# Optimization experiments

Hardware: AMD Instinct MI355X
Metric: run time of the kernel (lower is better)

The kernel has to match this reference:

```python
import jax, jax.numpy as jnp
import numpy as np

NUM_HEADS = 16
DIM = 1024
N_TOKENS = 2048
S0 = 8            # number of frames
P = N_TOKENS // S0  # tokens per frame
B = 1


def setup_inputs() -> dict:
    key = jax.random.key(0)
    ks = jax.random.split(key, 8)
    C = DIM
    x = jax.random.normal(ks[0], (B, N_TOKENS, C), dtype=jnp.float32)
    # nn.Linear-style weights (out_features, in_features), scaled ~1/sqrt(fan_in)
    Wqkv = jax.random.normal(ks[1], (3 * C, C), dtype=jnp.float32) * (C ** -0.5)
    bqkv = jnp.zeros((3 * C,), dtype=jnp.float32)
    Wproj = jax.random.normal(ks[2], (C, C), dtype=jnp.float32) * (C ** -0.5)
    bproj = jnp.zeros((C,), dtype=jnp.float32)
    frame_bias = jax.random.normal(ks[3], (S0, S0), dtype=jnp.float32) * 0.5
    # frame adjacency: random sparsity pattern, diagonal always allowed
    adj = jax.random.bernoulli(ks[4], 0.25, (S0, S0))
    adj = adj | jnp.eye(S0, dtype=bool)
    frame_ids = (jnp.arange(N_TOKENS) // P).astype(jnp.int64)
    is_hub = jax.random.bernoulli(ks[5], 0.05, (N_TOKENS,))
    return {
        'x': x, 'Wqkv': Wqkv, 'bqkv': bqkv, 'Wproj': Wproj, 'bproj': bproj,
        'frame_bias': frame_bias, 'adj': adj, 'frame_ids': frame_ids,
        'is_hub': is_hub,
    }


def _sparse_attention(x, Wqkv, bqkv, Wproj, bproj, frame_bias, adj, frame_ids, is_hub):
    Bx, N, C = x.shape
    H = NUM_HEADS
    D = C // H
    scale = D ** -0.5
    # qkv projection -> q,k,v each [B,H,N,D]
    qkv = x @ Wqkv.T + bqkv                      # [B,N,3C]
    qkv = qkv.reshape(Bx, N, 3, H, D).transpose(2, 0, 3, 1, 4)
    q, k, v = qkv[0], qkv[1], qkv[2]

    # token-level mask derived from frame-level structures (score_mod semantics)
    fi = frame_ids                               # [N]
    adj_allowed = adj[fi[:, None], fi[None, :]]  # [N,N] bool
    same_frame = fi[:, None] == fi[None, :]
    neither_hub = ~(is_hub[:, None] | is_hub[None, :])
    hub_allowed = same_frame | neither_hub       # mask_hub_tokens=True
    allowed = adj_allowed & hub_allowed
    bias = frame_bias[fi[:, None], fi[None, :]]  # soft_mask=True

    scores = jnp.einsum('bhqd,bhkd->bhqk', q, k) * scale
    scores = jnp.where(allowed, scores + bias, -jnp.inf)
    attn = jax.nn.softmax(scores, axis=-1)
    out = jnp.einsum('bhqk,bhkd->bhqd', attn, v)
    out = out.transpose(0, 2, 1, 3).reshape(Bx, N, C)
    return out @ Wproj.T + bproj


def reference(x, Wqkv, bqkv, Wproj, bproj, frame_bias, adj, frame_ids, is_hub):
    return _sparse_attention(x, Wqkv, bqkv, Wproj, bproj, frame_bias,
                             adj, frame_ids, is_hub)
```

## Files before the change

### kernel.cpp

```cpp
#include <hip/hip_runtime.h>
#include <hip/hip_bf16.h>
#include <math.h>

#define NTOK 2048
#define CDIM 1024
#define NHEAD 16
#define HDIM 64

typedef __attribute__((ext_vector_type(8))) short bf16x8;
typedef __attribute__((ext_vector_type(4))) short bf16x4;
typedef __attribute__((ext_vector_type(4))) float f32x4;
typedef __attribute__((ext_vector_type(4))) unsigned int u32x4;

__device__ inline unsigned short bf16_rn(float f) {
    unsigned int u = __float_as_uint(f);
    u += 0x7FFFu + ((u >> 16) & 1u);
    return (unsigned short)(u >> 16);
}

template <int N> __device__ inline void waitcnt_vm() {
    if constexpr (N == 0) asm volatile("s_waitcnt vmcnt(0)" ::: "memory");
    else if constexpr (N == 3) asm volatile("s_waitcnt vmcnt(3)" ::: "memory");
    else if constexpr (N == 4) asm volatile("s_waitcnt vmcnt(4)" ::: "memory");
}

__device__ inline void gload16(const void* g, void* l) {
    __builtin_amdgcn_global_load_lds((const __attribute__((address_space(1))) void*)g,
                                     (__attribute__((address_space(3))) void*)l,
                                     16, 0, 0);
}

__global__ __launch_bounds__(256) void conv3(const float* __restrict__ s0, unsigned short* __restrict__ h0, int nb0,
                                             const float* __restrict__ s1, unsigned short* __restrict__ h1, int nb1,
                                             const float* __restrict__ s2, unsigned short* __restrict__ h2) {
    int b = blockIdx.x;
    const float* s;
    unsigned short* hh;
    if (b < nb0) { s = s0; hh = h0; }
    else if (b < nb0 + nb1) { s = s1; hh = h1; b -= nb0; }
    else { s = s2; hh = h2; b -= nb0 + nb1; }
    const int i = b * 256 + threadIdx.x;
    float4 v = ((const float4*)s)[i];
    ushort4 h;
    h.x = bf16_rn(v.x); h.y = bf16_rn(v.y); h.z = bf16_rn(v.z); h.w = bf16_rn(v.w);
    ((ushort4*)hh)[i] = h;
}

template <int BM, int BN, int M, int N, int K, int MODE>
__global__ __launch_bounds__(256) void gemm_mfma(const unsigned short* __restrict__ Ah,
                                                 const unsigned short* __restrict__ Bh,
                                                 const float* __restrict__ bias,
                                                 float* __restrict__ C,
                                                 unsigned short* __restrict__ qg,
                                                 unsigned short* __restrict__ kg,
                                                 unsigned short* __restrict__ vtg) {
    constexpr int FM = BM / 32;
    constexpr int FN = BN / 32;
    constexpr int ASZ = BM * 32;
    constexpr int BSZ = BN * 32;
    constexpr int BUF = ASZ + BSZ;
    __shared__ unsigned short lds[2 * BUF];

    const int tid = threadIdx.x;
    const int lane = tid & 63;
    const int w = tid >> 6;
    const int m0 = blockIdx.y * BM;
    const int n0 = blockIdx.x * BN;
    const int wave_m = (w >> 1) * (BM / 2);
    const int wave_n = (w & 1) * (BN / 2);
    const int lr = lane & 15;
    const int kg_ = lane >> 4;
    const int srow = tid >> 2;
    const int scol = (tid & 3) * 8;

    const size_t aRow = (size_t)(m0 + srow) * K + scol;
    const size_t bRow = (size_t)(n0 + srow) * K + scol;

    f32x4 acc[FM][FN];
#pragma unroll
    for (int i = 0; i < FM; ++i)
#pragma unroll
        for (int j = 0; j < FN; ++j) acc[i][j] = {0.f, 0.f, 0.f, 0.f};

    auto stage = [&](int buf, int k0) {
        unsigned short* bb = lds + buf * BUF;
#pragma unroll
        for (int j = 0; j < BM / 64; ++j) {
            const size_t ga = aRow + (size_t)j * 64 * K + k0;
            gload16(Ah + ga, bb + (srow + j * 64) * 32 + scol);
        }
#pragma unroll
        for (int j = 0; j < BN / 64; ++j) {
            const size_t gb = bRow + (size_t)j * 64 * K + k0;
            gload16(Bh + gb, bb + ASZ + (srow + j * 64) * 32 + scol);
        }
    };

    stage(0, 0);
    constexpr int NL = BM / 64 + BN / 64;
    constexpr int NT = K / 32;
    for (int t = 0; t < NT; ++t) {
        const int cur = t & 1;
        if (t + 1 < NT) {
            stage(cur ^ 1, (t + 1) * 32);
            waitcnt_vm<NL>();
        } else {
            waitcnt_vm<0>();
        }
        __builtin_amdgcn_s_barrier();

        const unsigned short* bb = lds + cur * BUF;
        bf16x8 ah[FM], bh[FN];
#pragma unroll
        for (int f = 0; f < FM; ++f)
            ah[f] = *(const bf16x8*)&bb[(wave_m + f * 16 + lr) * 32 + kg_ * 8];
#pragma unroll
        for (int f = 0; f < FN; ++f)
            bh[f] = *(const bf16x8*)&bb[ASZ + (wave_n + f * 16 + lr) * 32 + kg_ * 8];
        __builtin_amdgcn_s_setprio(1);
#pragma unroll
        for (int fm = 0; fm < FM; ++fm)
#pragma unroll
            for (int fn = 0; fn < FN; ++fn)
                acc[fm][fn] = __builtin_amdgcn_mfma_f32_16x16x32_bf16(ah[fm], bh[fn], acc[fm][fn], 0, 0, 0);
        __builtin_amdgcn_s_setprio(0);
        asm volatile("" ::: "memory");
        __builtin_amdgcn_s_barrier();
    }

    if constexpr (MODE == 2) {
        float bv[FN];
#pragma unroll
        for (int fn = 0; fn < FN; ++fn) bv[fn] = bias[n0 + wave_n + fn * 16 + lr];
#pragma unroll
        for (int fm = 0; fm < FM; ++fm) {
            const int row0 = m0 + wave_m + fm * 16 + kg_ * 4;
#pragma unroll
            for (int fn = 0; fn < FN; ++fn) {
                const int col = n0 + wave_n + fn * 16 + lr;
#pragma unroll
                for (int r = 0; r < 4; ++r)
                    C[(size_t)(row0 + r) * N + col] = acc[fm][fn][r] + bv[fn];
            }
        }
    } else {
        const int reg = n0 >> 10;
#pragma unroll
        for (int fn = 0; fn < FN; ++fn) {
            const int col = n0 + wave_n + fn * 16 + lr;
            const int head = (col >> 6) & 15;
            const int d = col & 63;
            const float bv = bias[col];
#pragma unroll
            for (int fm = 0; fm < FM; ++fm) {
                const int row0 = m0 + wave_m + fm * 16 + kg_ * 4;
                if (reg == 2) {
                    ushort4 pk;
                    pk.x = bf16_rn(acc[fm][fn][0] + bv);
                    pk.y = bf16_rn(acc[fm][fn][1] + bv);
                    pk.z = bf16_rn(acc[fm][fn][2] + bv);
                    pk.w = bf16_rn(acc[fm][fn][3] + bv);
                    const size_t idx = (size_t)(head * 64 + d) * 2048 + (size_t)(row0 ^ ((d & 7) << 3));
                    *(ushort4*)&vtg[idx] = pk;
                } else {
                    const float sc = (reg == 0) ? 0.125f : 1.0f;
                    unsigned short* dp = (reg == 0) ? qg : kg;
#pragma unroll
                    for (int r = 0; r < 4; ++r) {
                        const int tok = row0 + r;
                        const size_t idx = ((size_t)head * 2048 + tok) * 64 + (d ^ ((tok & 7) << 3));
                        dp[idx] = bf16_rn((acc[fm][fn][r] + bv) * sc);
                    }
                }
            }
        }
    }
}

__global__ __launch_bounds__(512) void attn_mfma(const unsigned short* __restrict__ qg,
                                                 const unsigned short* __restrict__ kgb,
                                                 const unsigned short* __restrict__ vtg,
                                                 const float* __restrict__ frame_bias,
                                                 const int* __restrict__ adj,
                                                 const int* __restrict__ is_hub,
                                                 unsigned short* __restrict__ ath) {
    __shared__ unsigned short sBuf[2][2][2][64 * 64];
    __shared__ int sList[34];
    __shared__ float sFB[8];
    __shared__ unsigned long long sHub[32];
    __shared__ int sNT;

    const int bid = blockIdx.x;
    const int r8 = bid & 7, tt = bid >> 3;
    const int qb = tt & 31, hb = tt >> 5;
    const int h = r8 * 2 + hb;
    const int q0 = qb * 64;

    const int tid = threadIdx.x;
    const int lane = tid & 63;
    const int wq = tid >> 6;
    const int half = wq >> 2;
    const int lr = lane & 15;
    const int kg = lane >> 4;
    const int fi = q0 >> 8;

    const int qrow = (wq & 3) * 16 + lr;
    const int qgl = q0 + qrow;
    const unsigned short* qb_ = qg + ((size_t)h * 2048 + qgl) * 64;
    const int Xq = (qgl & 7) << 3;
    bf16x8 qh[2];
#pragma unroll
    for (int dc = 0; dc < 2; ++dc)
        qh[dc] = *(const bf16x8*)&qb_[(dc * 32 + kg * 8) ^ Xq];
    const bool hq = is_hub[qgl] != 0;

#pragma unroll
    for (int i = 0; i < 4; ++i) {
        const int t2 = wq * 4 + i;
        unsigned long long mb = __ballot(is_hub[t2 * 64 + lane] != 0);
        if (lane == 0) sHub[t2] = mb;
    }
    if (tid < 8) sFB[tid] = frame_bias[fi * 8 + tid];
    if (wq == 0) {
        const bool ok = (lane < 32) && (adj[fi * 8 + ((lane & 31) >> 2)] != 0);
        const unsigned long long am = __ballot(ok);
        if (lane == 0) {
            int c = 0;
#pragma unroll 1
            for (int t2 = 0; t2 < 32; ++t2)
                if ((am >> t2) & 1ull) sList[c++] = t2;
            sNT = c;
            sList[c] = sList[c - 1];
        }
    }
    __syncthreads();
    const int nt = sNT;
    const int npair = (nt + 1) >> 1;

    const int t256 = tid & 255;
    const int crow = t256 >> 3;
    const int ccol = (t256 & 7) * 8;
    const unsigned short* kbase = kgb + (size_t)h * 2048 * 64;
    const unsigned short* vbase = vtg + (size_t)h * 64 * 2048;

    auto stageOwn = [&](int buf, int n0s) {
        unsigned short* bk = &sBuf[buf][half][0][0];
        unsigned short* bv = &sBuf[buf][half][1][0];
        const int dst = t256 * 8;
        gload16(kbase + (size_t)(n0s + crow) * 64 + ccol, bk + dst);
        gload16(kbase + (size_t)(n0s + crow + 32) * 64 + ccol, bk + dst + 2048);
        gload16(vbase + (size_t)crow * 2048 + n0s + ccol, bv + dst);
        gload16(vbase + (size_t)(crow + 32) * 2048 + n0s + ccol, bv + dst + 2048);
    };

    float m_i = -INFINITY, l_i = 0.f;
    f32x4 oacc[4];
#pragma unroll
    for (int fd = 0; fd < 4; ++fd) oacc[fd] = {0.f, 0.f, 0.f, 0.f};

    stageOwn(0, sList[half] * 64);
#pragma unroll 1
    for (int p = 0; p < npair; ++p) {
        const int cur = p & 1;
        const int idx = 2 * p + half;
        if (p + 1 < npair) {
            stageOwn(cur ^ 1, sList[idx + 2] * 64);
            waitcnt_vm<4>();
        } else {
            waitcnt_vm<0>();
        }
        __builtin_amdgcn_s_barrier();

        const int tile = sList[idx];
        const bool live = idx < nt;
        const int fj = tile >> 2;
        const bool same = (fj == fi);
        const float biasv = sFB[fj];
        const unsigned long long hubmask = sHub[tile];
        const unsigned short* sKh = &sBuf[cur][half][0][0];
        const unsigned short* sVt = &sBuf[cur][half][1][0];

        f32x4 sacc[4];
#pragma unroll
        for (int fk = 0; fk < 4; ++fk) sacc[fk] = {0.f, 0.f, 0.f, 0.f};
        __builtin_amdgcn_s_setprio(1);
#pragma unroll
        for (int fk = 0; fk < 4; ++fk) {
            const int r = fk * 16 + lr;
            const int Xk = (r & 7) << 3;
            const int rb = r * 64;
#pragma unroll
            for (int dc = 0; dc < 2; ++dc) {
                bf16x8 khf = *(const bf16x8*)&sKh[rb + ((dc * 32 + kg * 8) ^ Xk)];
                sacc[fk] = __builtin_amdgcn_mfma_f32_16x16x32_bf16(khf, qh[dc], sacc[fk], 0, 0, 0);
            }
        }
        __builtin_amdgcn_s_setprio(0);

        float sv[4][4];
        float rmax = -INFINITY;
#pragma unroll
        for (int fk = 0; fk < 4; ++fk)
#pragma unroll
            for (int r = 0; r < 4; ++r) {
                float val = sacc[fk][r] + biasv;
                if (!same) {
                    const int k = fk * 16 + kg * 4 + r;
                    if (hq || ((hubmask >> k) & 1ull)) val = -INFINITY;
                }
                if (!live) val = -INFINITY;
                sv[fk][r] = val;
                rmax = fmaxf(rmax, val);
            }
        rmax = fmaxf(rmax, __shfl_xor(rmax, 16));
        rmax = fmaxf(rmax, __shfl_xor(rmax, 32));

        const float mn = fmaxf(m_i, rmax);
        const float alpha = (mn == -INFINITY) ? 1.f : __expf(m_i - mn);
        m_i = mn;

        float p4[4][4];
        float psum = 0.f;
#pragma unroll
        for (int fk = 0; fk < 4; ++fk)
#pragma unroll
            for (int r = 0; r < 4; ++r) {
                const float pv = (sv[fk][r] == -INFINITY) ? 0.f : __expf(sv[fk][r] - mn);
                p4[fk][r] = pv;
                psum += pv;
            }
        psum += __shfl_xor(psum, 16);
        psum += __shfl_xor(psum, 32);
        l_i = l_i * alpha + psum;
#pragma unroll
        for (int fd = 0; fd < 4; ++fd) {
            oacc[fd][0] *= alpha; oacc[fd][1] *= alpha;
            oacc[fd][2] *= alpha; oacc[fd][3] *= alpha;
        }

        unsigned int pc[4][2];
#pragma unroll
        for (int fk = 0; fk < 4; ++fk)
#pragma unroll
            for (int rp = 0; rp < 2; ++rp)
                pc[fk][rp] = (unsigned int)bf16_rn(p4[fk][2 * rp]) |
                             ((unsigned int)bf16_rn(p4[fk][2 * rp + 1]) << 16);
        __builtin_amdgcn_s_setprio(1);
#pragma unroll
        for (int c = 0; c < 2; ++c) {
            u32x4 pw = {pc[2 * c][0], pc[2 * c][1], pc[2 * c + 1][0], pc[2 * c + 1][1]};
            bf16x8 pbv = __builtin_bit_cast(bf16x8, pw);
#pragma unroll
            for (int fd = 0; fd < 4; ++fd) {
                const int vrow = fd * 16 + lr;
                const int Xv = (vrow & 7) << 3;
                const int vb = vrow * 64;
                bf16x4 v0 = *(const bf16x4*)&sVt[vb + ((c * 32 + kg * 4) ^ Xv)];
                bf16x4 v1 = *(const bf16x4*)&sVt[vb + ((c * 32 + 16 + kg * 4) ^ Xv)];
                bf16x8 va = __builtin_shufflevector(v0, v1, 0, 1, 2, 3, 4, 5, 6, 7);
                oacc[fd] = __builtin_amdgcn_mfma_f32_16x16x32_bf16(va, pbv, oacc[fd], 0, 0, 0);
            }
        }
        __builtin_amdgcn_s_setprio(0);
        asm volatile("" ::: "memory");
        __builtin_amdgcn_s_barrier();
    }

    float* mrg = (float*)&sBuf[0][0][0][0];
    const int mbase = ((wq & 3) * 64 + lane) * 18;
    if (half == 1) {
        mrg[mbase] = m_i;
        mrg[mbase + 1] = l_i;
#pragma unroll
        for (int fd = 0; fd < 4; ++fd)
#pragma unroll
            for (int r = 0; r < 4; ++r) mrg[mbase + 2 + fd * 4 + r] = oacc[fd][r];
    }
    __syncthreads();
    if (half == 0) {
        const float mb = mrg[mbase];
        const float lb = mrg[mbase + 1];
        const float m = fmaxf(m_i, mb);
        const float aa = (m_i == -INFINITY) ? 0.f : __expf(m_i - m);
        const float ab = (mb == -INFINITY) ? 0.f : __expf(mb - m);
        const float inv = 1.f / (l_i * aa + lb * ab);
#pragma unroll
        for (int fd = 0; fd < 4; ++fd) {
            ushort4 h4;
            unsigned short hs[4];
#pragma unroll
            for (int r = 0; r < 4; ++r) {
                const float o = (oacc[fd][r] * aa + mrg[mbase + 2 + fd * 4 + r] * ab) * inv;
                hs[r] = bf16_rn(o);
            }
            h4.x = hs[0]; h4.y = hs[1]; h4.z = hs[2]; h4.w = hs[3];
            const size_t idx = (size_t)qgl * CDIM + h * 64 + fd * 16 + kg * 4;
            *(ushort4*)&ath[idx] = h4;
        }
    }
}

extern "C" void kernel_launch(void* const* d_in, const int* in_sizes, int n_in,
                              void* d_out, int out_size, void* d_ws, size_t ws_size,
                              hipStream_t stream) {
    const float* x          = (const float*)d_in[0];
    const float* Wqkv       = (const float*)d_in[1];
    const float* bqkv       = (const float*)d_in[2];
    const float* Wproj      = (const float*)d_in[3];
    const float* bproj      = (const float*)d_in[4];
    const float* frame_bias = (const float*)d_in[5];
    const int*   adj        = (const int*)d_in[6];
    const int*   is_hub     = (const int*)d_in[8];
    float* out = (float*)d_out;

    char* ws = (char*)d_ws;
    size_t off = 0;
    auto alloc_us = [&](size_t n) { unsigned short* p = (unsigned short*)(ws + off); off += n * 2; return p; };
    unsigned short* qg  = alloc_us((size_t)NHEAD * NTOK * HDIM);
    unsigned short* kg  = alloc_us((size_t)NHEAD * NTOK * HDIM);
    unsigned short* vtg = alloc_us((size_t)NHEAD * HDIM * NTOK);
    unsigned short* xh  = alloc_us((size_t)NTOK * CDIM);
    unsigned short* wqh = alloc_us((size_t)3 * CDIM * CDIM);
    unsigned short* wph = alloc_us((size_t)CDIM * CDIM);
    unsigned short* ath = alloc_us((size_t)NTOK * CDIM);

    const int nb_x = (NTOK * CDIM / 4) / 256;
    const int nb_wq = (3 * CDIM * CDIM / 4) / 256;
    const int nb_wp = (CDIM * CDIM / 4) / 256;
    conv3<<<nb_x + nb_wq + nb_wp, 256, 0, stream>>>(x, xh, nb_x,
                                                    Wqkv, wqh, nb_wq,
                                                    Wproj, wph);

    gemm_mfma<64, 128, NTOK, 3 * CDIM, CDIM, 1>
        <<<dim3((3 * CDIM) / 128, NTOK / 64), 256, 0, stream>>>(
            xh, wqh, bqkv, nullptr, qg, kg, vtg);
    attn_mfma<<<512, 512, 0, stream>>>(qg, kg, vtg,
                                       frame_bias, adj, is_hub, ath);
    gemm_mfma<64, 128, NTOK, CDIM, CDIM, 2>
        <<<dim3(CDIM / 128, NTOK / 64), 256, 0, stream>>>(
            ath, wph, bproj, out, nullptr, nullptr, nullptr);
}
```

Baseline: 81.11 us.

## Split attention into 16-query blocks with per-wave key tiles and direct global loads

```diff
diff --git a/kernel.cpp b/kernel.cpp
--- a/kernel.cpp
+++ b/kernel.cpp
@@ -20,6 +20,7 @@
 
 template <int N> __device__ inline void waitcnt_vm() {
     if constexpr (N == 0) asm volatile("s_waitcnt vmcnt(0)" ::: "memory");
+    else if constexpr (N == 2) asm volatile("s_waitcnt vmcnt(2)" ::: "memory");
     else if constexpr (N == 3) asm volatile("s_waitcnt vmcnt(3)" ::: "memory");
     else if constexpr (N == 4) asm volatile("s_waitcnt vmcnt(4)" ::: "memory");
 }
@@ -51,8 +52,8 @@
                                                  const unsigned short* __restrict__ Bh,
                                                  const float* __restrict__ bias,
                                                  float* __restrict__ C,
-                                                 unsigned short* __restrict__ qg,
-                                                 unsigned short* __restrict__ kg,
+                                                 unsigned short* __restrict__ qgp,
+                                                 unsigned short* __restrict__ kgp,
                                                  unsigned short* __restrict__ vtg) {
     constexpr int FM = BM / 32;
     constexpr int FN = BN / 32;
@@ -74,7 +75,7 @@
     const int scol = (tid & 3) * 8;
 
     const size_t aRow = (size_t)(m0 + srow) * K + scol;
-    const size_t bRow = (size_t)(n0 + srow) * K + scol;
+    const size_t bRow = (size_t)(n0 + (srow & (BN - 1))) * K + scol;
 
     f32x4 acc[FM][FN];
 #pragma unroll
@@ -89,15 +90,17 @@
             const size_t ga = aRow + (size_t)j * 64 * K + k0;
             gload16(Ah + ga, bb + (srow + j * 64) * 32 + scol);
         }
-#pragma unroll
-        for (int j = 0; j < BN / 64; ++j) {
-            const size_t gb = bRow + (size_t)j * 64 * K + k0;
-            gload16(Bh + gb, bb + ASZ + (srow + j * 64) * 32 + scol);
+        if constexpr (BN >= 64) {
+#pragma unroll
+            for (int j = 0; j < (BN + 63) / 64; ++j) {
+                const size_t gb = bRow + (size_t)j * 64 * K + k0;
+                gload16(Bh + gb, bb + ASZ + ((srow & (BN - 1)) + j * 64) * 32 + scol);
+            }
         }
     };
 
     stage(0, 0);
-    constexpr int NL = BM / 64 + BN / 64;
+    constexpr int NL = BM / 64 + (BN + 63) / 64;
     constexpr int NT = K / 32;
     for (int t = 0; t < NT; ++t) {
         const int cur = t & 1;
@@ -164,7 +167,7 @@
                     *(ushort4*)&vtg[idx] = pk;
                 } else {
                     const float sc = (reg == 0) ? 0.125f : 1.0f;
-                    unsigned short* dp = (reg == 0) ? qg : kg;
+                    unsigned short* dp = (reg == 0) ? qgp : kgp;
 #pragma unroll
                     for (int r = 0; r < 4; ++r) {
                         const int tok = row0 + r;
@@ -177,36 +180,34 @@
     }
 }
 
-__global__ __launch_bounds__(512) void attn_mfma(const unsigned short* __restrict__ qg,
-                                                 const unsigned short* __restrict__ kgb,
+__global__ __launch_bounds__(256) void attn_mfma(const unsigned short* __restrict__ qgp,
+                                                 const unsigned short* __restrict__ kgp,
                                                  const unsigned short* __restrict__ vtg,
                                                  const float* __restrict__ frame_bias,
                                                  const int* __restrict__ adj,
                                                  const int* __restrict__ is_hub,
                                                  unsigned short* __restrict__ ath) {
-    __shared__ unsigned short sBuf[2][2][2][64 * 64];
-    __shared__ int sList[34];
+    __shared__ float sMrg[3][64][18];
+    __shared__ int sList[32];
     __shared__ float sFB[8];
     __shared__ unsigned long long sHub[32];
     __shared__ int sNT;
 
     const int bid = blockIdx.x;
     const int r8 = bid & 7, tt = bid >> 3;
-    const int qb = tt & 31, hb = tt >> 5;
+    const int q16 = tt & 127, hb = tt >> 7;
     const int h = r8 * 2 + hb;
-    const int q0 = qb * 64;
+    const int q0 = q16 * 16;
 
     const int tid = threadIdx.x;
     const int lane = tid & 63;
-    const int wq = tid >> 6;
-    const int half = wq >> 2;
+    const int w = tid >> 6;
     const int lr = lane & 15;
     const int kg = lane >> 4;
     const int fi = q0 >> 8;
 
-    const int qrow = (wq & 3) * 16 + lr;
-    const int qgl = q0 + qrow;
-    const unsigned short* qb_ = qg + ((size_t)h * 2048 + qgl) * 64;
+    const int qgl = q0 + lr;
+    const unsigned short* qb_ = qgp + ((size_t)h * 2048 + qgl) * 64;
     const int Xq = (qgl & 7) << 3;
     bf16x8 qh[2];
 #pragma unroll
@@ -215,13 +216,13 @@
     const bool hq = is_hub[qgl] != 0;
 
 #pragma unroll
-    for (int i = 0; i < 4; ++i) {
-        const int t2 = wq * 4 + i;
+    for (int i = 0; i < 8; ++i) {
+        const int t2 = w * 8 + i;
         unsigned long long mb = __ballot(is_hub[t2 * 64 + lane] != 0);
         if (lane == 0) sHub[t2] = mb;
     }
     if (tid < 8) sFB[tid] = frame_bias[fi * 8 + tid];
-    if (wq == 0) {
+    if (w == 0) {
         const bool ok = (lane < 32) && (adj[fi * 8 + ((lane & 31) >> 2)] != 0);
         const unsigned long long am = __ballot(ok);
         if (lane == 0) {
@@ -230,71 +231,55 @@
             for (int t2 = 0; t2 < 32; ++t2)
                 if ((am >> t2) & 1ull) sList[c++] = t2;
             sNT = c;
-            sList[c] = sList[c - 1];
         }
     }
     __syncthreads();
     const int nt = sNT;
-    const int npair = (nt + 1) >> 1;
-
-    const int t256 = tid & 255;
-    const int crow = t256 >> 3;
-    const int ccol = (t256 & 7) * 8;
-    const unsigned short* kbase = kgb + (size_t)h * 2048 * 64;
+
+    const unsigned short* kbase = kgp + (size_t)h * 2048 * 64;
     const unsigned short* vbase = vtg + (size_t)h * 64 * 2048;
-
-    auto stageOwn = [&](int buf, int n0s) {
-        unsigned short* bk = &sBuf[buf][half][0][0];
-        unsigned short* bv = &sBuf[buf][half][1][0];
-        const int dst = t256 * 8;
-        gload16(kbase + (size_t)(n0s + crow) * 64 + ccol, bk + dst);
-        gload16(kbase + (size_t)(n0s + crow + 32) * 64 + ccol, bk + dst + 2048);
-        gload16(vbase + (size_t)crow * 2048 + n0s + ccol, bv + dst);
-        gload16(vbase + (size_t)(crow + 32) * 2048 + n0s + ccol, bv + dst + 2048);
-    };
+    const int Xl = (lr & 7) << 3;
 
     float m_i = -INFINITY, l_i = 0.f;
     f32x4 oacc[4];
 #pragma unroll
     for (int fd = 0; fd < 4; ++fd) oacc[fd] = {0.f, 0.f, 0.f, 0.f};
 
-    stageOwn(0, sList[half] * 64);
 #pragma unroll 1
-    for (int p = 0; p < npair; ++p) {
-        const int cur = p & 1;
-        const int idx = 2 * p + half;
-        if (p + 1 < npair) {
-            stageOwn(cur ^ 1, sList[idx + 2] * 64);
-            waitcnt_vm<4>();
-        } else {
-            waitcnt_vm<0>();
-        }
-        __builtin_amdgcn_s_barrier();
-
-        const int tile = sList[idx];
-        const bool live = idx < nt;
+    for (int i = w; i < nt; i += 4) {
+        const int tile = sList[i];
+        const int n0s = tile * 64;
         const int fj = tile >> 2;
         const bool same = (fj == fi);
         const float biasv = sFB[fj];
         const unsigned long long hubmask = sHub[tile];
-        const unsigned short* sKh = &sBuf[cur][half][0][0];
-        const unsigned short* sVt = &sBuf[cur][half][1][0];
+
+        bf16x8 kf[4][2];
+#pragma unroll
+        for (int fk = 0; fk < 4; ++fk)
+#pragma unroll
+            for (int dc = 0; dc < 2; ++dc)
+                kf[fk][dc] = *(const bf16x8*)&kbase[(size_t)(n0s + fk * 16 + lr) * 64 +
+                                                   ((dc * 32 + kg * 8) ^ Xl)];
+        bf16x4 vf[2][4][2];
+#pragma unroll
+        for (int c = 0; c < 2; ++c)
+#pragma unroll
+            for (int fd = 0; fd < 4; ++fd) {
+                const size_t vb = (size_t)(fd * 16 + lr) * 2048 + n0s;
+                vf[c][fd][0] = *(const bf16x4*)&vbase[vb + ((c * 32 + kg * 4) ^ Xl)];
+                vf[c][fd][1] = *(const bf16x4*)&vbase[vb + ((c * 32 + 16 + kg * 4) ^ Xl)];
+            }
 
         f32x4 sacc[4];
 #pragma unroll
         for (int fk = 0; fk < 4; ++fk) sacc[fk] = {0.f, 0.f, 0.f, 0.f};
         __builtin_amdgcn_s_setprio(1);
 #pragma unroll
-        for (int fk = 0; fk < 4; ++fk) {
-            const int r = fk * 16 + lr;
-            const int Xk = (r & 7) << 3;
-            const int rb = r * 64;
-#pragma unroll
-            for (int dc = 0; dc < 2; ++dc) {
-                bf16x8 khf = *(const bf16x8*)&sKh[rb + ((dc * 32 + kg * 8) ^ Xk)];
-                sacc[fk] = __builtin_amdgcn_mfma_f32_16x16x32_bf16(khf, qh[dc], sacc[fk], 0, 0, 0);
-            }
-        }
+        for (int fk = 0; fk < 4; ++fk)
+#pragma unroll
+            for (int dc = 0; dc < 2; ++dc)
+                sacc[fk] = __builtin_amdgcn_mfma_f32_16x16x32_bf16(kf[fk][dc], qh[dc], sacc[fk], 0, 0, 0);
         __builtin_amdgcn_s_setprio(0);
 
         float sv[4][4];
@@ -308,7 +293,6 @@
                     const int k = fk * 16 + kg * 4 + r;
                     if (hq || ((hubmask >> k) & 1ull)) val = -INFINITY;
                 }
-                if (!live) val = -INFINITY;
                 sv[fk][r] = val;
                 rmax = fmaxf(rmax, val);
             }
@@ -352,48 +336,54 @@
             bf16x8 pbv = __builtin_bit_cast(bf16x8, pw);
 #pragma unroll
             for (int fd = 0; fd < 4; ++fd) {
-                const int vrow = fd * 16 + lr;
-                const int Xv = (vrow & 7) << 3;
-                const int vb = vrow * 64;
-                bf16x4 v0 = *(const bf16x4*)&sVt[vb + ((c * 32 + kg * 4) ^ Xv)];
-                bf16x4 v1 = *(const bf16x4*)&sVt[vb + ((c * 32 + 16 + kg * 4) ^ Xv)];
-                bf16x8 va = __builtin_shufflevector(v0, v1, 0, 1, 2, 3, 4, 5, 6, 7);
+                bf16x8 va = __builtin_shufflevector(vf[c][fd][0], vf[c][fd][1], 0, 1, 2, 3, 4, 5, 6, 7);
                 oacc[fd] = __builtin_amdgcn_mfma_f32_16x16x32_bf16(va, pbv, oacc[fd], 0, 0, 0);
             }
         }
         __builtin_amdgcn_s_setprio(0);
-        asm volatile("" ::: "memory");
-        __builtin_amdgcn_s_barrier();
-    }
-
-    float* mrg = (float*)&sBuf[0][0][0][0];
-    const int mbase = ((wq & 3) * 64 + lane) * 18;
-    if (half == 1) {
-        mrg[mbase] = m_i;
-        mrg[mbase + 1] = l_i;
+    }
+
+    __syncthreads();
+    if (w > 0) {
+        float* mp = &sMrg[w - 1][lane][0];
+        mp[0] = m_i;
+        mp[1] = l_i;
 #pragma unroll
         for (int fd = 0; fd < 4; ++fd)
 #pragma unroll
-            for (int r = 0; r < 4; ++r) mrg[mbase + 2 + fd * 4 + r] = oacc[fd][r];
+            for (int r = 0; r < 4; ++r) mp[2 + fd * 4 + r] = oacc[fd][r];
     }
     __syncthreads();
-    if (half == 0) {
-        const float mb = mrg[mbase];
-        const float lb = mrg[mbase + 1];
-        const float m = fmaxf(m_i, mb);
-        const float aa = (m_i == -INFINITY) ? 0.f : __expf(m_i - m);
-        const float ab = (mb == -INFINITY) ? 0.f : __expf(mb - m);
-        const float inv = 1.f / (l_i * aa + lb * ab);
+    if (w == 0) {
+        float m = m_i;
+#pragma unroll
+        for (int j = 0; j < 3; ++j) m = fmaxf(m, sMrg[j][lane][0]);
+        const float a0 = (m_i == -INFINITY) ? 0.f : __expf(m_i - m);
+        float lsum = l_i * a0;
+        float ov[4][4];
+#pragma unroll
+        for (int fd = 0; fd < 4; ++fd)
+#pragma unroll
+            for (int r = 0; r < 4; ++r) ov[fd][r] = oacc[fd][r] * a0;
+#pragma unroll
+        for (int j = 0; j < 3; ++j) {
+            const float mj = sMrg[j][lane][0];
+            const float aj = (mj == -INFINITY) ? 0.f : __expf(mj - m);
+            lsum += sMrg[j][lane][1] * aj;
+#pragma unroll
+            for (int fd = 0; fd < 4; ++fd)
+#pragma unroll
+                for (int r = 0; r < 4; ++r)
+                    ov[fd][r] += sMrg[j][lane][2 + fd * 4 + r] * aj;
+        }
+        const float inv = 1.f / lsum;
 #pragma unroll
         for (int fd = 0; fd < 4; ++fd) {
             ushort4 h4;
-            unsigned short hs[4];
-#pragma unroll
-            for (int r = 0; r < 4; ++r) {
-                const float o = (oacc[fd][r] * aa + mrg[mbase + 2 + fd * 4 + r] * ab) * inv;
-                hs[r] = bf16_rn(o);
-            }
-            h4.x = hs[0]; h4.y = hs[1]; h4.z = hs[2]; h4.w = hs[3];
+            h4.x = bf16_rn(ov[fd][0] * inv);
+            h4.y = bf16_rn(ov[fd][1] * inv);
+            h4.z = bf16_rn(ov[fd][2] * inv);
+            h4.w = bf16_rn(ov[fd][3] * inv);
             const size_t idx = (size_t)qgl * CDIM + h * 64 + fd * 16 + kg * 4;
             *(ushort4*)&ath[idx] = h4;
         }
@@ -434,9 +424,9 @@
     gemm_mfma<64, 128, NTOK, 3 * CDIM, CDIM, 1>
         <<<dim3((3 * CDIM) / 128, NTOK / 64), 256, 0, stream>>>(
             xh, wqh, bqkv, nullptr, qg, kg, vtg);
-    attn_mfma<<<512, 512, 0, stream>>>(qg, kg, vtg,
-                                       frame_bias, adj, is_hub, ath);
-    gemm_mfma<64, 128, NTOK, CDIM, CDIM, 2>
-        <<<dim3(CDIM / 128, NTOK / 64), 256, 0, stream>>>(
+    attn_mfma<<<2048, 256, 0, stream>>>(qg, kg, vtg,
+                                        frame_bias, adj, is_hub, ath);
+    gemm_mfma<64, 64, NTOK, CDIM, CDIM, 2>
+        <<<dim3(CDIM / 64, NTOK / 64), 256, 0, stream>>>(
             ath, wph, bproj, out, nullptr, nullptr, nullptr);
 }
```

Measured after the change: 96.41 us. 18.9% more time.
